# Kernel optimization log

Measured on AMD Instinct MI355X. Metric: run time of the kernel, lower is better.

Reference implementation:

```python
import jax, jax.numpy as jnp
import numpy as np

NUM_HEADS = 4
SCALE = 1.0  # source: self.scale = qkv_bias or head_dim**-0.5 -> True -> 1.0


def setup_inputs() -> dict:
    key = jax.random.key(0)
    ks = jax.random.split(key, 6)
    B_, N, C = 4096, 49, 128
    nW = 64
    return {
        "x": jax.random.normal(ks[0], (B_, N, C), dtype=jnp.float32),
        "mask": jax.random.normal(ks[1], (nW, N, N), dtype=jnp.float32),
        "w_qkv": jax.random.normal(ks[2], (C, 3 * C), dtype=jnp.float32) * (C ** -0.5),
        "b_qkv": jax.random.normal(ks[3], (3 * C,), dtype=jnp.float32) * 0.02,
        "w_proj": jax.random.normal(ks[4], (C, C), dtype=jnp.float32) * (C ** -0.5),
        "b_proj": jax.random.normal(ks[5], (C,), dtype=jnp.float32) * 0.02,
    }


def reference(x, mask, w_qkv, b_qkv, w_proj, b_proj):
    B_, N, C = x.shape
    H = NUM_HEADS
    hd = C // H
    # fused qkv projection: (B_, N, 3, H, hd) -> (3, B_, H, N, hd)
    qkv = (x @ w_qkv + b_qkv).reshape(B_, N, 3, H, hd).transpose(2, 0, 3, 1, 4)
    q, k, v = qkv[0], qkv[1], qkv[2]
    q = q * SCALE
    # per-window attention logits: (B_, H, N, N)
    attn = jnp.einsum("bhnd,bhmd->bhnm", q, k)
    nW = mask.shape[0]
    # additive window mask bias broadcast over batch and heads
    attn = attn.reshape(B_ // nW, nW, H, N, N) + mask[None, :, None, :, :]
    attn = jax.nn.softmax(attn, axis=-1).reshape(B_, H, N, N)
    out = jnp.einsum("bhnm,bhmd->bhnd", attn, v)  # (B_, H, N, hd)
    out = out.transpose(0, 2, 1, 3).reshape(B_, N, C)
    return out @ w_proj + b_proj
```

## Files before the change

kernel.cpp:

```cpp
#include <hip/hip_runtime.h>
#include <hip/hip_bf16.h>

typedef __attribute__((ext_vector_type(4))) float f32x4;
typedef _Float16 f16;
typedef __attribute__((ext_vector_type(8))) f16 f16x8;
typedef __attribute__((ext_vector_type(4))) f16 f16x4;
typedef __attribute__((ext_vector_type(2))) __fp16 fp16x2;

#define LDQ 136

#define GLOAD16(g, l)                                              \
  __builtin_amdgcn_global_load_lds(                                \
      (const __attribute__((address_space(1))) void*)(g),          \
      (__attribute__((address_space(3))) void*)(l), 16, 0, 0)

__global__ void pack_w_kernel(const float* __restrict__ w, f16* __restrict__ dst, int Ntot) {
  int idx = blockIdx.x * 256 + threadIdx.x;
  int total = (Ntot / 16) * 4 * 64;
  if (idx >= total) return;
  int lane = idx & 63;
  int kf = (idx >> 6) & 3;
  int nt = idx >> 8;
  int k0 = 32 * kf + 8 * (lane >> 4);
  int n = 16 * nt + (lane & 15);
  f16x8 v;
#pragma unroll
  for (int e = 0; e < 8; e++) v[e] = (f16)w[(k0 + e) * Ntot + n];
  *(f16x8*)(dst + (size_t)idx * 8) = v;
}

__global__ void pack_mask_kernel(const float* __restrict__ mask, float* __restrict__ dst) {
  int idx = blockIdx.x * 256 + threadIdx.x;
  int v = idx & 63;
  int l = (idx >> 6) & 63;
  int w = idx >> 12;
  int r = v & 3, mt = (v >> 2) & 3, nt = v >> 4;
  int q = 16 * nt + (l & 15);
  int key = 16 * mt + 4 * (l >> 4) + r;
  float val;
  if (key >= 49) val = -1e30f;
  else if (q < 49) val = mask[w * 2401 + q * 49 + key];
  else val = 0.f;
  dst[idx] = val;
}

__device__ __forceinline__ f16x4 pack4(f32x4 v) {
  union { f16x4 o; fp16x2 h[2]; } u;
  u.h[0] = __builtin_amdgcn_cvt_pkrtz(v[0], v[1]);
  u.h[1] = __builtin_amdgcn_cvt_pkrtz(v[2], v[3]);
  return u.o;
}

__device__ __forceinline__ f16x8 afrag(const float* xs, int row, int g0) {
  const f32x4 lo = *(const f32x4*)(xs + (((row << 5) + (g0 ^ (row & 7))) << 2));
  const f32x4 hi = *(const f32x4*)(xs + (((row << 5) + ((g0 + 1) ^ (row & 7))) << 2));
  union { f16x8 v; fp16x2 h[4]; } u;
  u.h[0] = __builtin_amdgcn_cvt_pkrtz(lo[0], lo[1]);
  u.h[1] = __builtin_amdgcn_cvt_pkrtz(lo[2], lo[3]);
  u.h[2] = __builtin_amdgcn_cvt_pkrtz(hi[0], hi[1]);
  u.h[3] = __builtin_amdgcn_cvt_pkrtz(hi[2], hi[3]);
  return u.v;
}

template <bool PM>
__global__ __launch_bounds__(256, 3) void winattn_fused(
    const float* __restrict__ x, const float* __restrict__ mask,
    const float* __restrict__ mask_p,
    const float* __restrict__ bqkv, const float* __restrict__ bproj,
    const f16* __restrict__ wqkv_p, const f16* __restrict__ wproj_p,
    float* __restrict__ out) {
  __shared__ float xs[64 * 128];
  f16* Os = (f16*)xs;

  const int tid = threadIdx.x;
  const int h = tid >> 6;
  const int l = tid & 63;
  const int lg = l >> 4;
  const int ll = l & 15;
  const int b = blockIdx.x;
  const float* xw = x + (size_t)b * 49 * 128;

#pragma unroll
  for (int i = 0; i < 8; i++) {
    int c = i * 256 + tid;
    int r = c >> 5, s = c & 31;
    float* lp = xs + c * 4;
    if (r < 49) {
      GLOAD16(xw + r * 128 + ((s ^ (r & 7)) << 2), lp);
    } else {
      *(f32x4*)lp = (f32x4){0.f, 0.f, 0.f, 0.f};
    }
  }
  __syncthreads();

  f16x4 qv[2][4];
  {
    f32x4 acc[2][4];
#pragma unroll
    for (int mi = 0; mi < 2; mi++)
#pragma unroll
      for (int t = 0; t < 4; t++) acc[mi][t] = (f32x4){0.f, 0.f, 0.f, 0.f};
#pragma unroll
    for (int kst = 0; kst < 4; kst++) {
      f16x8 wf0 = *(const f16x8*)(wqkv_p + (size_t)((((2 * h + 0) * 4 + kst) * 64) + l) * 8);
      f16x8 wf1 = *(const f16x8*)(wqkv_p + (size_t)((((2 * h + 1) * 4 + kst) * 64) + l) * 8);
#pragma unroll
      for (int t = 0; t < 4; t++) {
        f16x8 a = afrag(xs, 16 * t + ll, 8 * kst + 2 * lg);
        acc[0][t] = __builtin_amdgcn_mfma_f32_16x16x32_f16(wf0, a, acc[0][t], 0, 0, 0);
        acc[1][t] = __builtin_amdgcn_mfma_f32_16x16x32_f16(wf1, a, acc[1][t], 0, 0, 0);
      }
    }
#pragma unroll
    for (int mi = 0; mi < 2; mi++) {
      f32x4 bq = *(const f32x4*)(bqkv + 16 * (2 * h + mi) + 4 * lg);
#pragma unroll
      for (int t = 0; t < 4; t++) {
        f32x4 a = acc[mi][t];
#pragma unroll
        for (int r = 0; r < 4; r++) a[r] += bq[r];
        qv[mi][t] = pack4(a);
      }
    }
  }

  f16x4 kv[2][4];
  {
    f32x4 acc[2][4];
#pragma unroll
    for (int mi = 0; mi < 2; mi++)
#pragma unroll
      for (int t = 0; t < 4; t++) acc[mi][t] = (f32x4){0.f, 0.f, 0.f, 0.f};
#pragma unroll
    for (int kst = 0; kst < 4; kst++) {
      f16x8 wf0 = *(const f16x8*)(wqkv_p + (size_t)((((8 + 2 * h + 0) * 4 + kst) * 64) + l) * 8);
      f16x8 wf1 = *(const f16x8*)(wqkv_p + (size_t)((((8 + 2 * h + 1) * 4 + kst) * 64) + l) * 8);
#pragma unroll
      for (int t = 0; t < 4; t++) {
        f16x8 a = afrag(xs, 16 * t + ll, 8 * kst + 2 * lg);
        acc[0][t] = __builtin_amdgcn_mfma_f32_16x16x32_f16(wf0, a, acc[0][t], 0, 0, 0);
        acc[1][t] = __builtin_amdgcn_mfma_f32_16x16x32_f16(wf1, a, acc[1][t], 0, 0, 0);
      }
    }
#pragma unroll
    for (int mi = 0; mi < 2; mi++) {
      f32x4 bk = *(const f32x4*)(bqkv + 16 * (8 + 2 * h + mi) + 4 * lg);
#pragma unroll
      for (int t = 0; t < 4; t++) {
        f32x4 a = acc[mi][t];
#pragma unroll
        for (int r = 0; r < 4; r++) a[r] += bk[r];
        kv[mi][t] = pack4(a);
      }
    }
  }

  f16x4 vv[2][4];
  {
    f32x4 acc[2][4];
#pragma unroll
    for (int vi = 0; vi < 2; vi++)
#pragma unroll
      for (int t = 0; t < 4; t++) acc[vi][t] = (f32x4){0.f, 0.f, 0.f, 0.f};
#pragma unroll
    for (int kst = 0; kst < 4; kst++) {
      f16x8 wf0 = *(const f16x8*)(wqkv_p + (size_t)((((16 + 2 * h + 0) * 4 + kst) * 64) + l) * 8);
      f16x8 wf1 = *(const f16x8*)(wqkv_p + (size_t)((((16 + 2 * h + 1) * 4 + kst) * 64) + l) * 8);
#pragma unroll
      for (int t = 0; t < 4; t++) {
        f16x8 a = afrag(xs, 16 * t + ll, 8 * kst + 2 * lg);
        acc[0][t] = __builtin_amdgcn_mfma_f32_16x16x32_f16(a, wf0, acc[0][t], 0, 0, 0);
        acc[1][t] = __builtin_amdgcn_mfma_f32_16x16x32_f16(a, wf1, acc[1][t], 0, 0, 0);
      }
    }
#pragma unroll
    for (int vi = 0; vi < 2; vi++) {
      float bv = bqkv[16 * (16 + 2 * h + vi) + ll];
#pragma unroll
      for (int t = 0; t < 4; t++) {
        f32x4 a = acc[vi][t];
#pragma unroll
        for (int r = 0; r < 4; r++) a[r] += bv;
        vv[vi][t] = pack4(a);
      }
    }
  }
  __syncthreads();

  const f32x4* mp4 = PM ? (const f32x4*)(mask_p + (((size_t)(b & 63)) * 64 + l) * 64) : nullptr;
  const float* mk = mask + (size_t)(b & 63) * 49 * 49;
#pragma unroll
  for (int nt = 0; nt < 4; nt++) {
    f32x4 s[4];
#pragma unroll
    for (int mt = 0; mt < 4; mt++) {
      f32x4 c0;
      if (PM) c0 = mp4[nt * 4 + mt];
      else c0 = (f32x4){0.f, 0.f, 0.f, 0.f};
      c0 = __builtin_amdgcn_mfma_f32_16x16x16f16(kv[0][mt], qv[0][nt], c0, 0, 0, 0);
      s[mt] = __builtin_amdgcn_mfma_f32_16x16x16f16(kv[1][mt], qv[1][nt], c0, 0, 0, 0);
    }
    if (!PM) {
#pragma unroll
      for (int mt = 0; mt < 4; mt++)
#pragma unroll
        for (int r = 0; r < 4; r++) {
          int q = 16 * nt + ll;
          int key = 16 * mt + 4 * lg + r;
          float add;
          if (key >= 49) add = -1e30f;
          else if (q < 49) add = mk[q * 49 + key];
          else add = 0.f;
          s[mt][r] += add;
        }
    }
#pragma unroll
    for (int mt = 0; mt < 4; mt++)
#pragma unroll
      for (int r = 0; r < 4; r++) s[mt][r] = __expf(s[mt][r]);
    float sum = (((s[0][0] + s[0][1]) + (s[0][2] + s[0][3])) +
                 ((s[1][0] + s[1][1]) + (s[1][2] + s[1][3]))) +
                (((s[2][0] + s[2][1]) + (s[2][2] + s[2][3])) +
                 ((s[3][0] + s[3][1]) + (s[3][2] + s[3][3])));
    sum += __shfl_xor(sum, 16);
    sum += __shfl_xor(sum, 32);
    float invn = __builtin_amdgcn_rcpf(sum);
    f16x4 pb[4];
#pragma unroll
    for (int mt = 0; mt < 4; mt++) {
      f32x4 pv;
#pragma unroll
      for (int r = 0; r < 4; r++) pv[r] = s[mt][r] * invn;
      pb[mt] = pack4(pv);
    }
#pragma unroll
    for (int mi = 0; mi < 2; mi++) {
      f32x4 o = {0.f, 0.f, 0.f, 0.f};
#pragma unroll
      for (int c = 0; c < 4; c++)
        o = __builtin_amdgcn_mfma_f32_16x16x16f16(vv[mi][c], pb[c], o, 0, 0, 0);
      *(f16x4*)(&Os[(16 * nt + ll) * LDQ + 32 * h + 16 * mi + 4 * lg]) = pack4(o);
    }
  }
  __syncthreads();

  f16x8 of[4][4];
#pragma unroll
  for (int nt = 0; nt < 4; nt++)
#pragma unroll
    for (int kst = 0; kst < 4; kst++)
      of[nt][kst] = *(const f16x8*)(&Os[(16 * nt + ll) * LDQ + 32 * kst + 8 * lg]);
#pragma unroll
  for (int moi = 0; moi < 2; moi++) {
    int mo = 2 * h + moi;
    f16x8 wf2[4];
#pragma unroll
    for (int kst = 0; kst < 4; kst++)
      wf2[kst] = *(const f16x8*)(wproj_p + (size_t)(((mo * 4 + kst) * 64) + l) * 8);
    f32x4 bp = *(const f32x4*)(bproj + 16 * mo + 4 * lg);
#pragma unroll
    for (int nt = 0; nt < 4; nt++) {
      f32x4 acc = {0.f, 0.f, 0.f, 0.f};
#pragma unroll
      for (int kst = 0; kst < 4; kst++)
        acc = __builtin_amdgcn_mfma_f32_16x16x32_f16(wf2[kst], of[nt][kst], acc, 0, 0, 0);
#pragma unroll
      for (int r = 0; r < 4; r++) acc[r] += bp[r];
      int tok = 16 * nt + ll;
      if (tok < 49)
        *(f32x4*)(&out[((size_t)b * 49 + tok) * 128 + 16 * mo + 4 * lg]) = acc;
    }
  }
}

extern "C" void kernel_launch(void* const* d_in, const int* in_sizes, int n_in,
                              void* d_out, int out_size, void* d_ws, size_t ws_size,
                              hipStream_t stream) {
  const float* x = (const float*)d_in[0];
  const float* mask = (const float*)d_in[1];
  const float* wqkv = (const float*)d_in[2];
  const float* bqkv = (const float*)d_in[3];
  const float* wproj = (const float*)d_in[4];
  const float* bproj = (const float*)d_in[5];
  float* out = (float*)d_out;

  f16* wqkv_p = (f16*)d_ws;
  f16* wproj_p = wqkv_p + 24 * 4 * 64 * 8;
  float* mask_p = (float*)((char*)d_ws + 128 * 1024);

  const size_t need_pm = 128 * 1024 + 1048576;

  pack_w_kernel<<<24, 256, 0, stream>>>(wqkv, wqkv_p, 384);
  pack_w_kernel<<<8, 256, 0, stream>>>(wproj, wproj_p, 128);

  if (ws_size >= need_pm) {
    pack_mask_kernel<<<1024, 256, 0, stream>>>(mask, mask_p);
    winattn_fused<true><<<4096, 256, 0, stream>>>(x, mask, mask_p, bqkv, bproj, wqkv_p, wproj_p, out);
  } else {
    winattn_fused<false><<<4096, 256, 0, stream>>>(x, mask, nullptr, bqkv, bproj, wqkv_p, wproj_p, out);
  }
}
```

Baseline: 96.83 us.

## Convert staged x tile to fp16 in LDS once and raise occupancy

After the fp32 x tile is loaded into shared memory, all threads convert it once to an fp16 copy with a 16-way XOR swizzle and write it back in place. The QKV MFMA loops then read f16x8 fragments directly instead of reading two fp32 vectors and converting per fragment. Each QKV block now runs one output tile at a time, which cuts live accumulators, and launch bounds move from 3 to 4 blocks per CU. This removes a lot of repeated conversion ALU work and LDS traffic, at the cost of two extra barriers and possible register-spill pressure under the tighter bound.

```diff
diff --git a/kernel.cpp b/kernel.cpp
--- a/kernel.cpp
+++ b/kernel.cpp
@@ -44,16 +44,7 @@
   dst[idx] = val;
 }
 
-__device__ __forceinline__ f16x4 pack4(f32x4 v) {
-  union { f16x4 o; fp16x2 h[2]; } u;
-  u.h[0] = __builtin_amdgcn_cvt_pkrtz(v[0], v[1]);
-  u.h[1] = __builtin_amdgcn_cvt_pkrtz(v[2], v[3]);
-  return u.o;
-}
-
-__device__ __forceinline__ f16x8 afrag(const float* xs, int row, int g0) {
-  const f32x4 lo = *(const f32x4*)(xs + (((row << 5) + (g0 ^ (row & 7))) << 2));
-  const f32x4 hi = *(const f32x4*)(xs + (((row << 5) + ((g0 + 1) ^ (row & 7))) << 2));
+__device__ __forceinline__ f16x8 pack8(f32x4 lo, f32x4 hi) {
   union { f16x8 v; fp16x2 h[4]; } u;
   u.h[0] = __builtin_amdgcn_cvt_pkrtz(lo[0], lo[1]);
   u.h[1] = __builtin_amdgcn_cvt_pkrtz(lo[2], lo[3]);
@@ -62,14 +53,22 @@
   return u.v;
 }
 
+__device__ __forceinline__ f16x4 pack4(f32x4 v) {
+  union { f16x4 o; fp16x2 h[2]; } u;
+  u.h[0] = __builtin_amdgcn_cvt_pkrtz(v[0], v[1]);
+  u.h[1] = __builtin_amdgcn_cvt_pkrtz(v[2], v[3]);
+  return u.o;
+}
+
 template <bool PM>
-__global__ __launch_bounds__(256, 3) void winattn_fused(
+__global__ __launch_bounds__(256, 4) void winattn_fused(
     const float* __restrict__ x, const float* __restrict__ mask,
     const float* __restrict__ mask_p,
     const float* __restrict__ bqkv, const float* __restrict__ bproj,
     const f16* __restrict__ wqkv_p, const f16* __restrict__ wproj_p,
     float* __restrict__ out) {
   __shared__ float xs[64 * 128];
+  f16* xh = (f16*)xs;
   f16* Os = (f16*)xs;
 
   const int tid = threadIdx.x;
@@ -93,96 +92,101 @@
   }
   __syncthreads();
 
+  {
+    int row = tid >> 2;
+    int j0 = (tid & 3) << 2;
+    f16x8 cv[4];
+#pragma unroll
+    for (int k = 0; k < 4; k++) {
+      int j = j0 + k;
+      f32x4 lo = *(const f32x4*)(xs + ((row * 32 + ((2 * j) ^ (row & 7))) << 2));
+      f32x4 hi = *(const f32x4*)(xs + ((row * 32 + ((2 * j + 1) ^ (row & 7))) << 2));
+      cv[k] = pack8(lo, hi);
+    }
+    __syncthreads();
+#pragma unroll
+    for (int k = 0; k < 4; k++) {
+      int j = j0 + k;
+      *(f16x8*)(xh + row * 128 + ((j ^ (row & 15)) << 3)) = cv[k];
+    }
+    __syncthreads();
+  }
+
   f16x4 qv[2][4];
-  {
-    f32x4 acc[2][4];
-#pragma unroll
-    for (int mi = 0; mi < 2; mi++)
-#pragma unroll
-      for (int t = 0; t < 4; t++) acc[mi][t] = (f32x4){0.f, 0.f, 0.f, 0.f};
+#pragma unroll
+  for (int mi = 0; mi < 2; mi++) {
+    f32x4 acc[4];
+#pragma unroll
+    for (int t = 0; t < 4; t++) acc[t] = (f32x4){0.f, 0.f, 0.f, 0.f};
 #pragma unroll
     for (int kst = 0; kst < 4; kst++) {
-      f16x8 wf0 = *(const f16x8*)(wqkv_p + (size_t)((((2 * h + 0) * 4 + kst) * 64) + l) * 8);
-      f16x8 wf1 = *(const f16x8*)(wqkv_p + (size_t)((((2 * h + 1) * 4 + kst) * 64) + l) * 8);
+      f16x8 wf = *(const f16x8*)(wqkv_p + (size_t)((((2 * h + mi) * 4 + kst) * 64) + l) * 8);
 #pragma unroll
       for (int t = 0; t < 4; t++) {
-        f16x8 a = afrag(xs, 16 * t + ll, 8 * kst + 2 * lg);
-        acc[0][t] = __builtin_amdgcn_mfma_f32_16x16x32_f16(wf0, a, acc[0][t], 0, 0, 0);
-        acc[1][t] = __builtin_amdgcn_mfma_f32_16x16x32_f16(wf1, a, acc[1][t], 0, 0, 0);
+        int row = 16 * t + ll;
+        f16x8 a = *(const f16x8*)(xh + row * 128 + (((4 * kst + lg) ^ ll) << 3));
+        acc[t] = __builtin_amdgcn_mfma_f32_16x16x32_f16(wf, a, acc[t], 0, 0, 0);
       }
     }
-#pragma unroll
-    for (int mi = 0; mi < 2; mi++) {
-      f32x4 bq = *(const f32x4*)(bqkv + 16 * (2 * h + mi) + 4 * lg);
+    f32x4 bq = *(const f32x4*)(bqkv + 16 * (2 * h + mi) + 4 * lg);
+#pragma unroll
+    for (int t = 0; t < 4; t++) {
+      f32x4 a = acc[t];
+#pragma unroll
+      for (int r = 0; r < 4; r++) a[r] += bq[r];
+      qv[mi][t] = pack4(a);
+    }
+  }
+
+  f16x4 kv[2][4];
+#pragma unroll
+  for (int mi = 0; mi < 2; mi++) {
+    f32x4 acc[4];
+#pragma unroll
+    for (int t = 0; t < 4; t++) acc[t] = (f32x4){0.f, 0.f, 0.f, 0.f};
+#pragma unroll
+    for (int kst = 0; kst < 4; kst++) {
+      f16x8 wf = *(const f16x8*)(wqkv_p + (size_t)((((8 + 2 * h + mi) * 4 + kst) * 64) + l) * 8);
 #pragma unroll
       for (int t = 0; t < 4; t++) {
-        f32x4 a = acc[mi][t];
-#pragma unroll
-        for (int r = 0; r < 4; r++) a[r] += bq[r];
-        qv[mi][t] = pack4(a);
+        int row = 16 * t + ll;
+        f16x8 a = *(const f16x8*)(xh + row * 128 + (((4 * kst + lg) ^ ll) << 3));
+        acc[t] = __builtin_amdgcn_mfma_f32_16x16x32_f16(wf, a, acc[t], 0, 0, 0);
       }
     }
-  }
-
-  f16x4 kv[2][4];
-  {
-    f32x4 acc[2][4];
-#pragma unroll
-    for (int mi = 0; mi < 2; mi++)
-#pragma unroll
-      for (int t = 0; t < 4; t++) acc[mi][t] = (f32x4){0.f, 0.f, 0.f, 0.f};
+    f32x4 bk = *(const f32x4*)(bqkv + 16 * (8 + 2 * h + mi) + 4 * lg);
+#pragma unroll
+    for (int t = 0; t < 4; t++) {
+      f32x4 a = acc[t];
+#pragma unroll
+      for (int r = 0; r < 4; r++) a[r] += bk[r];
+      kv[mi][t] = pack4(a);
+    }
+  }
+
+  f16x4 vv[2][4];
+#pragma unroll
+  for (int vi = 0; vi < 2; vi++) {
+    f32x4 acc[4];
+#pragma unroll
+    for (int t = 0; t < 4; t++) acc[t] = (f32x4){0.f, 0.f, 0.f, 0.f};
 #pragma unroll
     for (int kst = 0; kst < 4; kst++) {
-      f16x8 wf0 = *(const f16x8*)(wqkv_p + (size_t)((((8 + 2 * h + 0) * 4 + kst) * 64) + l) * 8);
-      f16x8 wf1 = *(const f16x8*)(wqkv_p + (size_t)((((8 + 2 * h + 1) * 4 + kst) * 64) + l) * 8);
+      f16x8 wf = *(const f16x8*)(wqkv_p + (size_t)((((16 + 2 * h + vi) * 4 + kst) * 64) + l) * 8);
 #pragma unroll
       for (int t = 0; t < 4; t++) {
-        f16x8 a = afrag(xs, 16 * t + ll, 8 * kst + 2 * lg);
-        acc[0][t] = __builtin_amdgcn_mfma_f32_16x16x32_f16(wf0, a, acc[0][t], 0, 0, 0);
-        acc[1][t] = __builtin_amdgcn_mfma_f32_16x16x32_f16(wf1, a, acc[1][t], 0, 0, 0);
+        int row = 16 * t + ll;
+        f16x8 a = *(const f16x8*)(xh + row * 128 + (((4 * kst + lg) ^ ll) << 3));
+        acc[t] = __builtin_amdgcn_mfma_f32_16x16x32_f16(a, wf, acc[t], 0, 0, 0);
       }
     }
-#pragma unroll
-    for (int mi = 0; mi < 2; mi++) {
-      f32x4 bk = *(const f32x4*)(bqkv + 16 * (8 + 2 * h + mi) + 4 * lg);
-#pragma unroll
-      for (int t = 0; t < 4; t++) {
-        f32x4 a = acc[mi][t];
-#pragma unroll
-        for (int r = 0; r < 4; r++) a[r] += bk[r];
-        kv[mi][t] = pack4(a);
-      }
-    }
-  }
-
-  f16x4 vv[2][4];
-  {
-    f32x4 acc[2][4];
-#pragma unroll
-    for (int vi = 0; vi < 2; vi++)
-#pragma unroll
-      for (int t = 0; t < 4; t++) acc[vi][t] = (f32x4){0.f, 0.f, 0.f, 0.f};
-#pragma unroll
-    for (int kst = 0; kst < 4; kst++) {
-      f16x8 wf0 = *(const f16x8*)(wqkv_p + (size_t)((((16 + 2 * h + 0) * 4 + kst) * 64) + l) * 8);
-      f16x8 wf1 = *(const f16x8*)(wqkv_p + (size_t)((((16 + 2 * h + 1) * 4 + kst) * 64) + l) * 8);
-#pragma unroll
-      for (int t = 0; t < 4; t++) {
-        f16x8 a = afrag(xs, 16 * t + ll, 8 * kst + 2 * lg);
-        acc[0][t] = __builtin_amdgcn_mfma_f32_16x16x32_f16(a, wf0, acc[0][t], 0, 0, 0);
-        acc[1][t] = __builtin_amdgcn_mfma_f32_16x16x32_f16(a, wf1, acc[1][t], 0, 0, 0);
-      }
-    }
-#pragma unroll
-    for (int vi = 0; vi < 2; vi++) {
-      float bv = bqkv[16 * (16 + 2 * h + vi) + ll];
-#pragma unroll
-      for (int t = 0; t < 4; t++) {
-        f32x4 a = acc[vi][t];
-#pragma unroll
-        for (int r = 0; r < 4; r++) a[r] += bv;
-        vv[vi][t] = pack4(a);
-      }
+    float bv = bqkv[16 * (16 + 2 * h + vi) + ll];
+#pragma unroll
+    for (int t = 0; t < 4; t++) {
+      f32x4 a = acc[t];
+#pragma unroll
+      for (int r = 0; r < 4; r++) a[r] += bv;
+      vv[vi][t] = pack4(a);
     }
   }
   __syncthreads();
```

Result: no change. 95.70 us (-1.2%).
